# Kernel optimization log

Measured on AMD Instinct MI355X. Metric: run time of the kernel, lower is better.

Reference implementation:

```python
import jax, jax.numpy as jnp
import numpy as np

B, S, D, U = 32, 2048, 1024, 1024


def setup_inputs() -> dict:
    key = jax.random.key(0)
    ks = jax.random.split(key, 8)
    scale_in = 1.0 / np.sqrt(D)
    scale_u = 1.0 / np.sqrt(U)
    return {
        "query": jax.random.normal(ks[0], (B, D), dtype=jnp.float32),
        "values": jax.random.normal(ks[1], (B, S, D), dtype=jnp.float32),
        "W1": jax.random.normal(ks[2], (D, U), dtype=jnp.float32) * scale_in,
        "b1": jnp.zeros((U,), dtype=jnp.float32),
        "W2": jax.random.normal(ks[3], (D, U), dtype=jnp.float32) * scale_in,
        "b2": jnp.zeros((U,), dtype=jnp.float32),
        "V": jax.random.normal(ks[4], (U, 1), dtype=jnp.float32) * scale_u,
        "bV": jnp.zeros((1,), dtype=jnp.float32),
    }


def reference(query, values, W1, b1, W2, b2, V, bV):
    # values: [B, S, D] -> [B, S, U]; query: [B, D] -> [B, 1, U]
    proj_v = jnp.einsum("bsd,du->bsu", values, W1) + b1
    proj_q = (query @ W2 + b2)[:, None, :]
    # score: [B, S, 1]
    score = jnp.einsum("bsu,uo->bso", jnp.tanh(proj_v + proj_q), V) + bV
    attention_weights = jax.nn.softmax(score, axis=1)
    # context: [B, D]
    context_vector = jnp.sum(attention_weights * values, axis=1)
    return (context_vector, attention_weights)
```

## Files before the change

kernel.cpp:

```cpp
#include <hip/hip_runtime.h>

#define DEVFN __device__ __forceinline__
#define GLOBAL_AS __attribute__((address_space(1)))
#define LDS_AS __attribute__((address_space(3)))

typedef __attribute__((ext_vector_type(4))) float f32x4;
typedef __attribute__((ext_vector_type(8))) short short8;
typedef __attribute__((ext_vector_type(8))) unsigned short ushort8;

constexpr int CB = 32;
constexpr int CS = 2048;
constexpr int CD = 1024;
constexpr int CU = 1024;
constexpr int CM = CB * CS;

DEVFN unsigned f2bf_u(float f) {
    unsigned u = __float_as_uint(f);
    return (u + 0x7FFFu + ((u >> 16) & 1u)) >> 16;
}
DEVFN unsigned f2bf_pack(float lo, float hi) {
    return f2bf_u(lo) | (f2bf_u(hi) << 16);
}
DEVFN float tanh_fast(float x) {
    float e = exp2f(x * 2.885390081777927f);
    return 1.0f - 2.0f * __builtin_amdgcn_rcpf(e + 1.0f);
}

__global__ void k_bias1(const float* __restrict__ q, const float* __restrict__ W2,
                        float* __restrict__ bpart) {
    int dc = blockIdx.x, b = blockIdx.y;
    int t = threadIdx.x;
    __shared__ float qs[128];
    if (t < 128) qs[t] = q[b * CD + dc * 128 + t];
    __syncthreads();
    float acc0 = 0.f, acc1 = 0.f, acc2 = 0.f, acc3 = 0.f;
    const float* w2 = W2 + (size_t)(dc * 128) * CU + t;
#pragma unroll 4
    for (int d = 0; d < 128; ++d) {
        float qv = qs[d];
        const float* r = w2 + (size_t)d * CU;
        acc0 += qv * r[0];
        acc1 += qv * r[256];
        acc2 += qv * r[512];
        acc3 += qv * r[768];
    }
    float* o = bpart + (size_t)(b * 8 + dc) * CU + t;
    o[0] = acc0; o[256] = acc1; o[512] = acc2; o[768] = acc3;
}

__global__ void k_bias2(const float* __restrict__ bpart, const float* __restrict__ b1,
                        const float* __restrict__ b2, float* __restrict__ bias) {
    int idx = blockIdx.x * 256 + threadIdx.x;
    int b = idx >> 10, u = idx & 1023;
    float s = b1[u] + b2[u];
#pragma unroll
    for (int dc = 0; dc < 8; ++dc) s += bpart[(size_t)(b * 8 + dc) * CU + u];
    bias[idx] = s;
}

__global__ void k_packW1(const float* __restrict__ W1, unsigned short* __restrict__ W1p) {
    int tid = blockIdx.x * 256 + threadIdx.x;
    int o8  = tid * 8;
    int l   = (o8 >> 3) & 63;
    int ub  = (o8 >> 9) & 15;
    int ut  = (o8 >> 13) & 3;
    int kt  = o8 >> 15;
    int u  = ut * 256 + ub * 16 + (l & 15);
    int d0 = kt * 32 + (l >> 4) * 8;
    ushort8 v;
#pragma unroll
    for (int j = 0; j < 8; ++j)
        v[j] = (unsigned short)f2bf_u(W1[(size_t)(d0 + j) * CU + u]);
    *(ushort8*)(W1p + o8) = v;
}

__global__ __launch_bounds__(512, 2) void k_score(
    const float* __restrict__ values, const unsigned short* __restrict__ W1p,
    const float* __restrict__ bias, const float* __restrict__ V,
    float* __restrict__ score) {
    __shared__ __align__(16) char smem[8192];

    const int t = threadIdx.x;
    const int w = t >> 6, l = t & 63;
    const int m0 = blockIdx.x * 64;
    const int bb = m0 >> 11;

    const float* aSrcT = values + (size_t)(m0 + (t >> 3)) * CD + (t & 7) * 4;
    const int aWrByte = (t >> 7) * 1024
                      + (((((t >> 3) & 15) ^ ((t & 7) >> 1)) | (((t & 7) >> 1) << 4)) << 4)
                      + (t & 1) * 8;
    const int aRdOff = ((((l & 15) ^ (l >> 4)) | ((l >> 4) << 4)) << 4);
    const unsigned short* bSrc = W1p + (size_t)w * 4096 + l * 8;

    f32x4 zero4 = {0.f, 0.f, 0.f, 0.f};
    f32x4 acc[4][8];
#pragma unroll
    for (int i = 0; i < 4; ++i)
#pragma unroll
        for (int j = 0; j < 8; ++j) acc[i][j] = zero4;

    short8 bFA[8], bFB[8];
    f32x4 aH0, aH1;

    {
#pragma unroll
        for (int jj = 0; jj < 8; ++jj)
            bFA[jj] = *(const short8*)(bSrc + jj * 512);
        aH0 = __builtin_nontemporal_load((const f32x4*)aSrcT);
        aH1 = __builtin_nontemporal_load((const f32x4*)(aSrcT + 32));
        uint2 pk;
        pk.x = f2bf_pack(aH0[0], aH0[1]);
        pk.y = f2bf_pack(aH0[2], aH0[3]);
        *(uint2*)(smem + aWrByte) = pk;
        asm volatile("s_waitcnt lgkmcnt(0)" ::: "memory");
        asm volatile("s_barrier" ::: "memory");
    }

#define SCORE_BODY(KT, BF_CUR, BF_NXT, AH_LD, AH_WR, DO_LDB, DO_LDA, DO_WR)        \
    {                                                                               \
        if (DO_LDB) {                                                               \
            const unsigned short* bs = bSrc + (size_t)((KT) + 1) * 32768;           \
            _Pragma("unroll")                                                       \
            for (int jj = 0; jj < 8; ++jj)                                          \
                BF_NXT[jj] = *(const short8*)(bs + jj * 512);                       \
        }                                                                           \
        if (DO_LDA)                                                                 \
            AH_LD = __builtin_nontemporal_load(                                     \
                (const f32x4*)(aSrcT + ((KT) + 2) * 32));                           \
        const char* aB = smem + ((KT) & 1) * 4096;                                  \
        short8 aF[4];                                                               \
        _Pragma("unroll")                                                           \
        for (int i = 0; i < 4; ++i)                                                 \
            aF[i] = *(const short8*)(aB + i * 1024 + aRdOff);                       \
        __builtin_amdgcn_s_setprio(1);                                              \
        _Pragma("unroll")                                                           \
        for (int i = 0; i < 4; ++i)                                                 \
            _Pragma("unroll")                                                       \
            for (int j = 0; j < 8; ++j)                                             \
                acc[i][j] = __builtin_amdgcn_mfma_f32_16x16x32_bf16(                \
                    aF[i], BF_CUR[j], acc[i][j], 0, 0, 0);                          \
        __builtin_amdgcn_s_setprio(0);                                              \
        if (DO_WR) {                                                                \
            uint2 pk;                                                               \
            pk.x = f2bf_pack(AH_WR[0], AH_WR[1]);                                   \
            pk.y = f2bf_pack(AH_WR[2], AH_WR[3]);                                   \
            *(uint2*)(smem + (((KT) + 1) & 1) * 4096 + aWrByte) = pk;               \
        }                                                                           \
        asm volatile("s_waitcnt lgkmcnt(0)" ::: "memory");                          \
        asm volatile("s_barrier" ::: "memory");                                     \
    }

    for (int kt = 0; kt < 30; kt += 2) {
        SCORE_BODY(kt,     bFA, bFB, aH0, aH1, 1, 1, 1)
        SCORE_BODY(kt + 1, bFB, bFA, aH1, aH0, 1, 1, 1)
    }
    SCORE_BODY(30, bFA, bFB, aH0, aH1, 1, 0, 1)
    SCORE_BODY(31, bFB, bFA, aH1, aH0, 0, 0, 0)
#undef SCORE_BODY

    float part[4][4];
#pragma unroll
    for (int i = 0; i < 4; ++i)
#pragma unroll
        for (int rr = 0; rr < 4; ++rr) part[i][rr] = 0.f;

#pragma unroll
    for (int j = 0; j < 8; ++j) {
        int col = w * 128 + j * 16 + (l & 15);
        float vv = V[col];
        float bz = bias[bb * CU + col];
#pragma unroll
        for (int i = 0; i < 4; ++i)
#pragma unroll
            for (int rr = 0; rr < 4; ++rr)
                part[i][rr] += vv * tanh_fast(acc[i][j][rr] + bz);
    }

    __syncthreads();
    float* red = (float*)smem;
#pragma unroll
    for (int i = 0; i < 4; ++i)
#pragma unroll
        for (int rr = 0; rr < 4; ++rr) {
            float v = part[i][rr];
            v += __shfl_xor(v, 1);
            v += __shfl_xor(v, 2);
            v += __shfl_xor(v, 4);
            v += __shfl_xor(v, 8);
            if ((l & 15) == 0)
                red[w * 64 + i * 16 + (l >> 4) * 4 + rr] = v;
        }
    __syncthreads();
    if (t < 64) {
        float s = 0.f;
#pragma unroll
        for (int ww = 0; ww < 8; ++ww) s += red[ww * 64 + t];
        score[m0 + t] = s;
    }
}

__global__ void k_softmax(const float* __restrict__ score, float* __restrict__ wts) {
    int b = blockIdx.x, t = threadIdx.x;
    int i0 = b * CS + t, i1 = i0 + 1024;
    float s0 = score[i0];
    float s1 = score[i1];
    __shared__ float red[16];
    int wv = t >> 6, ln = t & 63;
    float m = fmaxf(s0, s1);
#pragma unroll
    for (int o = 32; o >= 1; o >>= 1) m = fmaxf(m, __shfl_xor(m, o));
    if (ln == 0) red[wv] = m;
    __syncthreads();
    float M = red[0];
#pragma unroll
    for (int k = 1; k < 16; ++k) M = fmaxf(M, red[k]);
    float e0 = __expf(s0 - M), e1 = __expf(s1 - M);
    float sm = e0 + e1;
#pragma unroll
    for (int o = 32; o >= 1; o >>= 1) sm += __shfl_xor(sm, o);
    __syncthreads();
    if (ln == 0) red[wv] = sm;
    __syncthreads();
    float T = 0.f;
#pragma unroll
    for (int k = 0; k < 16; ++k) T += red[k];
    float inv = 1.0f / T;
    wts[i0] = e0 * inv;
    wts[i1] = e1 * inv;
}

__global__ void k_ctx_part(const float* __restrict__ values, const float* __restrict__ wts,
                           float* __restrict__ part) {
    int b = blockIdx.y, sc = blockIdx.x;
    int t = threadIdx.x;
    const float* vb = values + ((size_t)b * CS + sc * 64) * CD + t * 4;
    const float* wb = wts + b * CS + sc * 64;
    f32x4 a = {0.f, 0.f, 0.f, 0.f};
#pragma unroll 8
    for (int s = 0; s < 64; ++s) {
        float wgt = wb[s];
        f32x4 v = *(const f32x4*)(vb + (size_t)s * CD);
        a += v * wgt;
    }
    *(f32x4*)(part + (size_t)(b * 32 + sc) * CD + t * 4) = a;
}

__global__ void k_ctx_red(const float* __restrict__ part, float* __restrict__ ctx) {
    int idx = blockIdx.x * 256 + threadIdx.x;
    int b = idx >> 10, d = idx & 1023;
    float s = 0.f;
#pragma unroll 8
    for (int c = 0; c < 32; ++c) s += part[(size_t)(b * 32 + c) * CD + d];
    ctx[idx] = s;
}

extern "C" void kernel_launch(void* const* d_in, const int* in_sizes, int n_in,
                              void* d_out, int out_size, void* d_ws, size_t ws_size,
                              hipStream_t stream) {
    const float* query  = (const float*)d_in[0];
    const float* values = (const float*)d_in[1];
    const float* W1     = (const float*)d_in[2];
    const float* b1     = (const float*)d_in[3];
    const float* W2     = (const float*)d_in[4];
    const float* b2     = (const float*)d_in[5];
    const float* V      = (const float*)d_in[6];

    float* out = (float*)d_out;
    float* ctx = out;
    float* wts = out + 32768;

    char* ws = (char*)d_ws;
    float*          score = (float*)ws;
    float*          bias  = (float*)(ws + (1 << 20));
    unsigned short* W1p   = (unsigned short*)(ws + (1 << 20) + (1 << 17));
    float*          part  = (float*)(ws + (1 << 20) + (1 << 17) + (1 << 21));
    float*          bpart = part;

    k_bias1<<<dim3(8, 32), 256, 0, stream>>>(query, W2, bpart);
    k_bias2<<<128, 256, 0, stream>>>(bpart, b1, b2, bias);
    k_packW1<<<512, 256, 0, stream>>>(W1, W1p);
    k_score<<<1024, 512, 0, stream>>>(values, W1p, bias, V, score);
    k_softmax<<<32, 1024, 0, stream>>>(score, wts);
    k_ctx_part<<<dim3(32, 32), 256, 0, stream>>>(values, wts, part);
    k_ctx_red<<<128, 256, 0, stream>>>(part, ctx);
}
```

Baseline: 221.6 us.

## Fuse partial context and local softmax stats into score kernel via LDS-resident tile

The score kernel now keeps every bf16 K-slice of its 64-row values tile in a large LDS buffer instead of double-buffering. After computing scores, each block works out a local max and exp-sum, then a weighted partial context from the LDS copy. The final reduction kernel rescales the partials with those per-block stats, in flash-attention style. This removes the separate context kernel's second full fp32 read of values. In exchange, the roughly 130 KB LDS footprint limits occupancy to one block per CU, and the context is now computed from bf16-rounded values.

```diff
diff --git a/kernel.cpp b/kernel.cpp
--- a/kernel.cpp
+++ b/kernel.cpp
@@ -1,12 +1,11 @@
 #include <hip/hip_runtime.h>
 
 #define DEVFN __device__ __forceinline__
-#define GLOBAL_AS __attribute__((address_space(1)))
-#define LDS_AS __attribute__((address_space(3)))
 
 typedef __attribute__((ext_vector_type(4))) float f32x4;
+typedef __attribute__((ext_vector_type(2))) float f32x2;
 typedef __attribute__((ext_vector_type(8))) short short8;
-typedef __attribute__((ext_vector_type(8))) unsigned short ushort8;
+typedef __attribute__((ext_vector_type(2))) unsigned short ushort2v;
 
 constexpr int CB = 32;
 constexpr int CS = 2048;
@@ -20,6 +19,12 @@
 }
 DEVFN unsigned f2bf_pack(float lo, float hi) {
     return f2bf_u(lo) | (f2bf_u(hi) << 16);
+}
+DEVFN uint2 cvt4(f32x4 a) {
+    uint2 r;
+    r.x = f2bf_pack(a[0], a[1]);
+    r.y = f2bf_pack(a[2], a[3]);
+    return r;
 }
 DEVFN float tanh_fast(float x) {
     float e = exp2f(x * 2.885390081777927f);
@@ -58,7 +63,8 @@
     bias[idx] = s;
 }
 
-__global__ void k_packW1(const float* __restrict__ W1, unsigned short* __restrict__ W1p) {
+__global__ void k_packW1(const float* __restrict__ W1,
+                         unsigned short* __restrict__ W1p) {
     int tid = blockIdx.x * 256 + threadIdx.x;
     int o8  = tid * 8;
     int l   = (o8 >> 3) & 63;
@@ -67,18 +73,22 @@
     int kt  = o8 >> 15;
     int u  = ut * 256 + ub * 16 + (l & 15);
     int d0 = kt * 32 + (l >> 4) * 8;
-    ushort8 v;
+    unsigned short vv[8];
 #pragma unroll
     for (int j = 0; j < 8; ++j)
-        v[j] = (unsigned short)f2bf_u(W1[(size_t)(d0 + j) * CU + u]);
-    *(ushort8*)(W1p + o8) = v;
+        vv[j] = (unsigned short)f2bf_u(W1[(size_t)(d0 + j) * CU + u]);
+    short8 v;
+#pragma unroll
+    for (int j = 0; j < 8; ++j) v[j] = (short)vv[j];
+    *(short8*)(W1p + o8) = v;
 }
 
 __global__ __launch_bounds__(512, 2) void k_score(
     const float* __restrict__ values, const unsigned short* __restrict__ W1p,
     const float* __restrict__ bias, const float* __restrict__ V,
-    float* __restrict__ score) {
-    __shared__ __align__(16) char smem[8192];
+    float* __restrict__ score, float* __restrict__ partc,
+    float2* __restrict__ mstats) {
+    __shared__ __align__(16) char smem[133632];
 
     const int t = threadIdx.x;
     const int w = t >> 6, l = t & 63;
@@ -86,18 +96,17 @@
     const int bb = m0 >> 11;
 
     const float* aSrcT = values + (size_t)(m0 + (t >> 3)) * CD + (t & 7) * 4;
-    const int aWrByte = (t >> 7) * 1024
-                      + (((((t >> 3) & 15) ^ ((t & 7) >> 1)) | (((t & 7) >> 1) << 4)) << 4)
-                      + (t & 1) * 8;
-    const int aRdOff = ((((l & 15) ^ (l >> 4)) | ((l >> 4) << 4)) << 4);
-    const unsigned short* bSrc = W1p + (size_t)w * 4096 + l * 8;
-
-    f32x4 zero4 = {0.f, 0.f, 0.f, 0.f};
+    const int llw = ((t >> 3) & 15) | (((t >> 1) & 3) << 4);
+    const int aWr = (t >> 7) * 1024 + ((llw ^ (((llw >> 4) & 3) << 1)) << 4)
+                  + (t & 1) * 8;
+    const int aRd = (l ^ (((l >> 4) & 3) << 1)) << 4;
+    const unsigned short* bSrc = W1p + w * 4096 + l * 8;
+
     f32x4 acc[4][8];
 #pragma unroll
     for (int i = 0; i < 4; ++i)
 #pragma unroll
-        for (int j = 0; j < 8; ++j) acc[i][j] = zero4;
+        for (int j = 0; j < 8; ++j) acc[i][j] = f32x4{0.f, 0.f, 0.f, 0.f};
 
     short8 bFA[8], bFB[8];
     f32x4 aH0, aH1;
@@ -107,11 +116,8 @@
         for (int jj = 0; jj < 8; ++jj)
             bFA[jj] = *(const short8*)(bSrc + jj * 512);
         aH0 = __builtin_nontemporal_load((const f32x4*)aSrcT);
+        *(uint2*)(smem + aWr) = cvt4(aH0);
         aH1 = __builtin_nontemporal_load((const f32x4*)(aSrcT + 32));
-        uint2 pk;
-        pk.x = f2bf_pack(aH0[0], aH0[1]);
-        pk.y = f2bf_pack(aH0[2], aH0[3]);
-        *(uint2*)(smem + aWrByte) = pk;
         asm volatile("s_waitcnt lgkmcnt(0)" ::: "memory");
         asm volatile("s_barrier" ::: "memory");
     }
@@ -127,11 +133,11 @@
         if (DO_LDA)                                                                 \
             AH_LD = __builtin_nontemporal_load(                                     \
                 (const f32x4*)(aSrcT + ((KT) + 2) * 32));                           \
-        const char* aB = smem + ((KT) & 1) * 4096;                                  \
+        const char* aB = smem + (KT) * 4096;                                        \
         short8 aF[4];                                                               \
         _Pragma("unroll")                                                           \
         for (int i = 0; i < 4; ++i)                                                 \
-            aF[i] = *(const short8*)(aB + i * 1024 + aRdOff);                       \
+            aF[i] = *(const short8*)(aB + i * 1024 + aRd);                          \
         __builtin_amdgcn_s_setprio(1);                                              \
         _Pragma("unroll")                                                           \
         for (int i = 0; i < 4; ++i)                                                 \
@@ -140,12 +146,8 @@
                 acc[i][j] = __builtin_amdgcn_mfma_f32_16x16x32_bf16(                \
                     aF[i], BF_CUR[j], acc[i][j], 0, 0, 0);                          \
         __builtin_amdgcn_s_setprio(0);                                              \
-        if (DO_WR) {                                                                \
-            uint2 pk;                                                               \
-            pk.x = f2bf_pack(AH_WR[0], AH_WR[1]);                                   \
-            pk.y = f2bf_pack(AH_WR[2], AH_WR[3]);                                   \
-            *(uint2*)(smem + (((KT) + 1) & 1) * 4096 + aWrByte) = pk;               \
-        }                                                                           \
+        if (DO_WR)                                                                  \
+            *(uint2*)(smem + ((KT) + 1) * 4096 + aWr) = cvt4(AH_WR);                \
         asm volatile("s_waitcnt lgkmcnt(0)" ::: "memory");                          \
         asm volatile("s_barrier" ::: "memory");                                     \
     }
@@ -166,9 +168,9 @@
 
 #pragma unroll
     for (int j = 0; j < 8; ++j) {
-        int col = w * 128 + j * 16 + (l & 15);
-        float vv = V[col];
-        float bz = bias[bb * CU + col];
+        const int col = w * 128 + j * 16 + (l & 15);
+        const float vv = V[col];
+        const float bz = bias[bb * CU + col];
 #pragma unroll
         for (int i = 0; i < 4; ++i)
 #pragma unroll
@@ -176,8 +178,9 @@
                 part[i][rr] += vv * tanh_fast(acc[i][j][rr] + bz);
     }
 
-    __syncthreads();
-    float* red = (float*)smem;
+    float* red    = (float*)(smem + 131072);
+    float* scores = (float*)(smem + 133120);
+    float* ps     = (float*)(smem + 133376);
 #pragma unroll
     for (int i = 0; i < 4; ++i)
 #pragma unroll
@@ -196,6 +199,36 @@
 #pragma unroll
         for (int ww = 0; ww < 8; ++ww) s += red[ww * 64 + t];
         score[m0 + t] = s;
+        scores[t] = s;
+    }
+    __syncthreads();
+
+    float mloc = scores[0];
+#pragma unroll 8
+    for (int s = 1; s < 64; ++s) mloc = fmaxf(mloc, scores[s]);
+    if (t < 64) ps[t] = __expf(scores[t] - mloc);
+    __syncthreads();
+    if (t == 0) {
+        float den = 0.f;
+#pragma unroll 8
+        for (int s = 0; s < 64; ++s) den += ps[s];
+        mstats[blockIdx.x] = float2{mloc, den};
+    }
+    {
+        const int c  = t * 2;
+        const int u  = (c >> 3) & 3;
+        const int xr = u << 1;
+        const int cB = (c >> 5) * 4096 + u * 256 + (c & 7) * 2;
+        float c0 = 0.f, c1 = 0.f;
+#pragma unroll 8
+        for (int s = 0; s < 64; ++s) {
+            float wg = ps[s];
+            const int addr = cB + (s >> 4) * 1024 + (((s & 15) ^ xr) << 4);
+            ushort2v uv = *(const ushort2v*)(smem + addr);
+            c0 += wg * __uint_as_float((unsigned)uv[0] << 16);
+            c1 += wg * __uint_as_float((unsigned)uv[1] << 16);
+        }
+        *(f32x2*)(partc + (size_t)blockIdx.x * CD + c) = f32x2{c0, c1};
     }
 }
 
@@ -229,29 +262,23 @@
     wts[i1] = e1 * inv;
 }
 
-__global__ void k_ctx_part(const float* __restrict__ values, const float* __restrict__ wts,
-                           float* __restrict__ part) {
-    int b = blockIdx.y, sc = blockIdx.x;
-    int t = threadIdx.x;
-    const float* vb = values + ((size_t)b * CS + sc * 64) * CD + t * 4;
-    const float* wb = wts + b * CS + sc * 64;
-    f32x4 a = {0.f, 0.f, 0.f, 0.f};
-#pragma unroll 8
-    for (int s = 0; s < 64; ++s) {
-        float wgt = wb[s];
-        f32x4 v = *(const f32x4*)(vb + (size_t)s * CD);
-        a += v * wgt;
-    }
-    *(f32x4*)(part + (size_t)(b * 32 + sc) * CD + t * 4) = a;
-}
-
-__global__ void k_ctx_red(const float* __restrict__ part, float* __restrict__ ctx) {
+__global__ void k_ctx_red(const float* __restrict__ partc,
+                          const float2* __restrict__ mstats,
+                          float* __restrict__ ctx) {
     int idx = blockIdx.x * 256 + threadIdx.x;
     int b = idx >> 10, d = idx & 1023;
-    float s = 0.f;
+    const float2* ms = mstats + b * 32;
+    float M = ms[0].x;
 #pragma unroll 8
-    for (int c = 0; c < 32; ++c) s += part[(size_t)(b * 32 + c) * CD + d];
-    ctx[idx] = s;
+    for (int k = 1; k < 32; ++k) M = fmaxf(M, ms[k].x);
+    float num = 0.f, den = 0.f;
+#pragma unroll 4
+    for (int k = 0; k < 32; ++k) {
+        float g = __expf(ms[k].x - M);
+        num += g * partc[(size_t)(b * 32 + k) * CD + d];
+        den += g * ms[k].y;
+    }
+    ctx[idx] = num / den;
 }
 
 extern "C" void kernel_launch(void* const* d_in, const int* in_sizes, int n_in,
@@ -270,17 +297,17 @@
     float* wts = out + 32768;
 
     char* ws = (char*)d_ws;
-    float*          score = (float*)ws;
-    float*          bias  = (float*)(ws + (1 << 20));
-    unsigned short* W1p   = (unsigned short*)(ws + (1 << 20) + (1 << 17));
-    float*          part  = (float*)(ws + (1 << 20) + (1 << 17) + (1 << 21));
-    float*          bpart = part;
+    float*          score  = (float*)ws;
+    float*          bias   = (float*)(ws + (1 << 20));
+    unsigned short* W1p    = (unsigned short*)(ws + (1 << 20) + (1 << 17));
+    float*          partc  = (float*)(ws + (1 << 20) + (1 << 17) + (1 << 21));
+    float2*         mstats = (float2*)(ws + (1 << 20) + (1 << 17) + (1 << 21) + (4 << 20));
+    float*          bpart  = partc;
 
     k_bias1<<<dim3(8, 32), 256, 0, stream>>>(query, W2, bpart);
     k_bias2<<<128, 256, 0, stream>>>(bpart, b1, b2, bias);
     k_packW1<<<512, 256, 0, stream>>>(W1, W1p);
-    k_score<<<1024, 512, 0, stream>>>(values, W1p, bias, V, score);
+    k_score<<<1024, 512, 0, stream>>>(values, W1p, bias, V, score, partc, mstats);
     k_softmax<<<32, 1024, 0, stream>>>(score, wts);
-    k_ctx_part<<<dim3(32, 32), 256, 0, stream>>>(values, wts, part);
-    k_ctx_red<<<128, 256, 0, stream>>>(part, ctx);
-}
+    k_ctx_red<<<128, 256, 0, stream>>>(partc, mstats, ctx);
+}
```

Measured after the change: 230.2 us. +3.9%, slower.
